# Kernel optimization log

Measured on AMD Instinct MI355X. Metric: run time of the kernel, lower is better.

The kernel has to match this reference:

```python
import jax, jax.numpy as jnp
import numpy as np

N0, N1, N2 = 100000, 20000, 4000   # src(block0), dst(block0)=src(block1), dst(block1)
R = 3                               # number of relations
E0, E1 = 160000, 64000              # edges per relation per block
IN_FEATS, HID = 128, 128
TSS, RS = 64, 64
NTOT = 200000                       # global node count for tss/rs embed tables
F_IN = HID + TSS + RS               # IGConv input feature dim = 256


def _lin(key, fi, fo):
    k1, k2 = jax.random.split(key)
    s = float(1.0 / np.sqrt(fi))
    w = jax.random.uniform(k1, (fi, fo), minval=-s, maxval=s, dtype=jnp.float32)
    b = jax.random.uniform(k2, (fo,), minval=-s, maxval=s, dtype=jnp.float32)
    return w, b


def setup_inputs() -> dict:
    ks = jax.random.split(jax.random.key(0), 32)
    inp = {}
    inp["x_user"] = jax.random.normal(ks[0], (N0, IN_FEATS), dtype=jnp.float32)
    inp["tss_embed"] = jax.random.normal(ks[1], (NTOT, TSS), dtype=jnp.float32)
    inp["rs_embed"] = jax.random.normal(ks[2], (NTOT, RS), dtype=jnp.float32)
    inp["src_nid0"] = jax.random.randint(ks[3], (N0,), 0, NTOT)
    inp["src_nid1"] = jax.random.randint(ks[4], (N1,), 0, NTOT)
    inp["e0_src"] = jax.random.randint(ks[5], (R, E0), 0, N0)
    inp["e0_dst"] = jax.random.randint(ks[6], (R, E0), 0, N1)
    inp["e1_src"] = jax.random.randint(ks[7], (R, E1), 0, N1)
    inp["e1_dst"] = jax.random.randint(ks[8], (R, E1), 0, N2)
    inp["embed_w"], inp["embed_b"] = _lin(ks[9], IN_FEATS, HID)
    i = 10
    for l in (1, 2):
        for nm, fi in (("fc1", F_IN), ("fc2", 3 * F_IN), ("fc3", 2 * HID)):
            pw, pb = zip(*[_lin(jax.random.fold_in(ks[i], r), fi, HID) for r in range(R)])
            inp["l%d_%s_w" % (l, nm)] = jnp.stack(pw)  # [R, fi, HID]
            inp["l%d_%s_b" % (l, nm)] = jnp.stack(pb)  # [R, HID]
            i += 1
    inp["attn_w1"], inp["attn_b1"] = _lin(ks[i], HID, HID)
    inp["attn_w2"] = _lin(ks[i + 1], HID, 1)[0]  # Linear(hid,1,bias=False)
    inp["pred_w"], inp["pred_b"] = _lin(ks[i + 2], HID, 1)
    return inp


def _igconv(src_feat, dst_feat, esrc, edst, n_dst, fc1w, fc1b, fc2w, fc2b, fc3w, fc3b):
    # copy_u gather then max/mean/sum segment reductions over destination nodes
    m = src_feat[esrc]                                   # [E, F]
    s = jax.ops.segment_sum(m, edst, num_segments=n_dst)
    deg = jax.ops.segment_sum(jnp.ones(esrc.shape, m.dtype), edst, num_segments=n_dst)
    mean = s / jnp.maximum(deg, 1.0)[:, None]
    mx = jax.ops.segment_max(m, edst, num_segments=n_dst)
    mx = jnp.where(deg[:, None] > 0, mx, jnp.zeros_like(mx))  # DGL zeros for isolated dst
    msg = jnp.concatenate([mx, mean, s], axis=1)         # [n_dst, 3F]
    inp = jnp.concatenate([msg @ fc2w + fc2b, dst_feat @ fc1w + fc1b], axis=1)
    return jax.nn.relu(inp) @ fc3w + fc3b                # [n_dst, HID]


def _attn(z, w1, b1, w2):
    # SemanticAttention: z [N, R, HID]
    w = (jnp.tanh(z @ w1 + b1) @ w2).mean(0)             # [R, 1]
    beta = jax.nn.softmax(w, axis=0)                     # [R, 1]
    return (beta[None] * z).sum(1)                       # [N, HID]


def _forward(x_user, tss_embed, rs_embed, embed_w, embed_b,
             l1_fc1_w, l1_fc1_b, l1_fc2_w, l1_fc2_b, l1_fc3_w, l1_fc3_b,
             l2_fc1_w, l2_fc1_b, l2_fc2_w, l2_fc2_b, l2_fc3_w, l2_fc3_b,
             attn_w1, attn_b1, attn_w2, pred_w, pred_b,
             src_nid0, src_nid1, e0_src, e0_dst, e1_src, e1_dst):
    u0 = x_user @ embed_w + embed_b                      # self.embed
    feat0 = jnp.concatenate([u0, tss_embed[src_nid0], rs_embed[src_nid0]], axis=1)  # [N0,256]
    conv1 = jax.vmap(lambda es, ed, w1, b1, w2, b2, w3, b3:
                     _igconv(feat0, feat0[:N1], es, ed, N1, w1, b1, w2, b2, w3, b3))
    z1 = conv1(e0_src, e0_dst, l1_fc1_w, l1_fc1_b, l1_fc2_w, l1_fc2_b, l1_fc3_w, l1_fc3_b)  # [R,N1,HID]
    h1 = jax.nn.relu(_attn(jnp.transpose(z1, (1, 0, 2)), attn_w1, attn_b1, attn_w2))  # [N1,HID]
    feat1 = jnp.concatenate([h1, tss_embed[src_nid1], rs_embed[src_nid1]], axis=1)    # [N1,256]
    conv2 = jax.vmap(lambda es, ed, w1, b1, w2, b2, w3, b3:
                     _igconv(feat1, feat1[:N2], es, ed, N2, w1, b1, w2, b2, w3, b3))
    z2 = conv2(e1_src, e1_dst, l2_fc1_w, l2_fc1_b, l2_fc2_w, l2_fc2_b, l2_fc3_w, l2_fc3_b)  # [R,N2,HID]
    h2 = _attn(jnp.transpose(z2, (1, 0, 2)), attn_w1, attn_b1, attn_w2)              # [N2,HID]
    return jax.nn.sigmoid(h2 @ pred_w + pred_b)          # [N2,1]


def reference(x_user, tss_embed, rs_embed, src_nid0, src_nid1,
              e0_src, e0_dst, e1_src, e1_dst, embed_w, embed_b,
              l1_fc1_w, l1_fc1_b, l1_fc2_w, l1_fc2_b, l1_fc3_w, l1_fc3_b,
              l2_fc1_w, l2_fc1_b, l2_fc2_w, l2_fc2_b, l2_fc3_w, l2_fc3_b,
              attn_w1, attn_b1, attn_w2, pred_w, pred_b):
    return _forward(x_user, tss_embed, rs_embed, embed_w, embed_b,
                    l1_fc1_w, l1_fc1_b, l1_fc2_w, l1_fc2_b, l1_fc3_w, l1_fc3_b,
                    l2_fc1_w, l2_fc1_b, l2_fc2_w, l2_fc2_b, l2_fc3_w, l2_fc3_b,
                    attn_w1, attn_b1, attn_w2, pred_w, pred_b,
                    src_nid0, src_nid1, e0_src, e0_dst, e1_src, e1_dst)
```

## Files before the change

### kernel.cpp

```cpp
#include <hip/hip_runtime.h>
#include <math.h>


typedef short s16x8 __attribute__((ext_vector_type(8)));
typedef float f32x4 __attribute__((ext_vector_type(4)));

__device__ __forceinline__ ushort f2bf(float f) {
  unsigned u = __float_as_uint(f);
  return (ushort)((u + 0x7FFFu + ((u >> 16) & 1u)) >> 16);
}
__device__ __forceinline__ float bf2f(unsigned hbits) {
  return __uint_as_float(hbits << 16);
}
__device__ __forceinline__ unsigned pack2(float lo, float hi) {
  return (unsigned)f2bf(lo) | ((unsigned)f2bf(hi) << 16);
}

struct PrepAll {
  const float* src[8];
  ushort* dst[8];
  int K[8];
  int total[8];
};

__global__ __launch_bounds__(256) void prep_all(PrepAll P)
{
  int t = blockIdx.z;
  int off = blockIdx.x * 256 + threadIdx.x;
  if (off >= P.total[t]) return;
  int K = P.K[t];
  int k = off % K;
  int n = (off / K) & 127;
  int r = off / (K * 128);
  P.dst[t][off] = f2bf(P.src[t][((size_t)r * K + k) * 128 + n]);
}

struct GemmDesc {
  const void* A; int lda; size_t aStride; int aKind;
  const ushort* Wt; size_t wStride;
  const float* bias; int biasStride;
  void* C; int ldc; size_t cStride; int cKind;
  int M, K, relu;
  const ushort* aggM; const ushort* aggS; const float* invdeg;
  size_t aggStride; int invStride;
  const int* gnid; const float* gtss; const float* grs;
};

template<int AKIND>
__device__ __forceinline__ uint4 loadA(const void* Ab, const ushort* AgM,
                                       const ushort* AgS, int lda, int row,
                                       bool rowOK, int k0, int quad, float idg)
{
  uint4 pk = make_uint4(0u, 0u, 0u, 0u);
  if (rowOK) {
    if constexpr (AKIND == 1) {
      pk = *(const uint4*)((const ushort*)Ab + (size_t)row * lda + k0 + quad * 8);
    } else if constexpr (AKIND == 0) {
      const float* A32 = (const float*)Ab;
      float4 fa = *(const float4*)(A32 + (size_t)row * lda + k0 + quad * 8);
      float4 fb = *(const float4*)(A32 + (size_t)row * lda + k0 + quad * 8 + 4);
      pk.x = pack2(fa.x, fa.y); pk.y = pack2(fa.z, fa.w);
      pk.z = pack2(fb.x, fb.y); pk.w = pack2(fb.z, fb.w);
    } else {
      int seg = k0 >> 8;
      int jj  = (k0 & 255) + quad * 8;
      const ushort* Ag = (seg == 0) ? AgM : AgS;
      pk = *(const uint4*)(Ag + (size_t)row * 256 + jj);
      if (seg == 1) {
        pk.x = pack2(bf2f(pk.x & 0xFFFFu) * idg, bf2f(pk.x >> 16) * idg);
        pk.y = pack2(bf2f(pk.y & 0xFFFFu) * idg, bf2f(pk.y >> 16) * idg);
        pk.z = pack2(bf2f(pk.z & 0xFFFFu) * idg, bf2f(pk.z >> 16) * idg);
        pk.w = pack2(bf2f(pk.w & 0xFFFFu) * idg, bf2f(pk.w >> 16) * idg);
      }
    }
  }
  return pk;
}

template<int K, int AKIND>
__device__ __forceinline__ void gemm_core(const GemmDesc& d, int r, ushort* Bs)
{
  constexpr int NC = K / 64;
  constexpr int NF = K / 32;

  const int tid = threadIdx.x;
  const int wave = tid >> 6, lane = tid & 63;
  const int m16 = lane & 15, quad = lane >> 4;
  const int rowBase = blockIdx.x * 64;
  const int row = rowBase + wave * 16 + m16;
  const bool rowOK = row < d.M;
  const ushort* Wt = d.Wt + (size_t)r * d.wStride;

  const void* Ab = (const char*)d.A +
      (size_t)r * d.aStride * (AKIND == 0 ? sizeof(float) : sizeof(ushort));
  const ushort* AgM = d.aggM + (size_t)r * d.aggStride;
  const ushort* AgS = d.aggS + (size_t)r * d.aggStride;

  float idg = 1.f;
  if (AKIND == 2 && rowOK) idg = d.invdeg[(size_t)r * d.invStride + row];

  f32x4 acc[8];
  #pragma unroll
  for (int j = 0; j < 8; ++j)
    #pragma unroll
    for (int p = 0; p < 4; ++p) acc[j][p] = 0.f;

  uint4 pkAll[(K <= 256) ? NF : 2];
  if constexpr (K <= 256) {
    #pragma unroll
    for (int f = 0; f < NF; ++f)
      pkAll[f] = loadA<AKIND>(Ab, AgM, AgS, d.lda, row, rowOK, f * 32, quad, idg);
  }

  #pragma unroll
  for (int c = 0; c < NC; ++c) {
    if constexpr (K > 256) {
      pkAll[0] = loadA<AKIND>(Ab, AgM, AgS, d.lda, row, rowOK, c * 64,      quad, idg);
      pkAll[1] = loadA<AKIND>(Ab, AgM, AgS, d.lda, row, rowOK, c * 64 + 32, quad, idg);
    }
    if (c) __syncthreads();
    #pragma unroll
    for (int i = 0; i < 4; ++i) {
      int q = tid + 256 * i;
      int col = ((q >> 6) & 7) * 16 + (q & 15);
      int kk  = c * 64 + (q >> 9) * 32 + ((q >> 4) & 3) * 8;
      *(uint4*)&Bs[q * 8] = *(const uint4*)(Wt + (size_t)col * K + kk);
    }
    __syncthreads();

    #pragma unroll
    for (int ks = 0; ks < 2; ++ks) {
      uint4 pk = (K <= 256) ? pkAll[c * 2 + ks] : pkAll[ks];
      s16x8 af = *(s16x8*)&pk;
      #pragma unroll
      for (int j = 0; j < 8; ++j) {
        s16x8 bf = *(const s16x8*)&Bs[((ks * 8 + j) * 64 + lane) * 8];
        acc[j] = __builtin_amdgcn_mfma_f32_16x16x32_bf16(af, bf, acc[j], 0, 0, 0);
      }
    }
  }

  const float* bias = d.bias + (size_t)r * d.biasStride;
  float bcol[8];
  #pragma unroll
  for (int j = 0; j < 8; ++j) bcol[j] = bias[j * 16 + m16];

  #pragma unroll
  for (int p = 0; p < 4; ++p) {
    int grow = rowBase + wave * 16 + quad * 4 + p;
    if (grow >= d.M) continue;
    if (d.cKind == 0) {
      float* Crow = (float*)d.C + (size_t)r * d.cStride + (size_t)grow * d.ldc;
      #pragma unroll
      for (int j = 0; j < 8; ++j) {
        float v = acc[j][p] + bcol[j];
        if (d.relu) v = fmaxf(v, 0.f);
        Crow[j * 16 + m16] = v;
      }
    } else {
      ushort* Crow = (ushort*)d.C + (size_t)r * d.cStride + (size_t)grow * d.ldc;
      #pragma unroll
      for (int j = 0; j < 8; ++j) {
        float v = acc[j][p] + bcol[j];
        if (d.relu) v = fmaxf(v, 0.f);
        Crow[j * 16 + m16] = f2bf(v);
      }
    }
  }

  if constexpr (K == 128) {
    if (d.gnid) {
      #pragma unroll
      for (int i = 0; i < 8; ++i) {
        int q = tid + 256 * i;
        int grow = rowBase + (q >> 5);
        int c = q & 31;
        if (grow >= d.M) continue;
        int id = d.gnid[grow];
        float4 v = (c < 16) ? *(const float4*)(d.gtss + (size_t)id * 64 + c * 4)
                            : *(const float4*)(d.grs  + (size_t)id * 64 + (c - 16) * 4);
        uint2 g; g.x = pack2(v.x, v.y); g.y = pack2(v.z, v.w);
        *(uint2*)((ushort*)d.C + (size_t)grow * d.ldc + 128 + c * 4) = g;
      }
    }
  }
}

__global__ __launch_bounds__(256, 4) void gemm_mfma(GemmDesc d0, GemmDesc d1)
{
  __shared__ __align__(16) ushort Bs[1024 * 8];
  const GemmDesc& d = blockIdx.z ? d1 : d0;
  const int r = blockIdx.y;
  if (d.K == 128)      gemm_core<128, 0>(d, r, Bs);
  else if (d.K == 256) gemm_core<256, 1>(d, r, Bs);
  else                 gemm_core<768, 2>(d, r, Bs);
}

__global__ __launch_bounds__(256, 4) void attn_mfma(
    const float* __restrict__ z, const ushort* __restrict__ w1t,
    const float* __restrict__ b1, const float* __restrict__ w2,
    int N, float* __restrict__ wsum)
{
  const int r = blockIdx.y;
  const float* zr = z + (size_t)r * N * 128;
  __shared__ __align__(16) ushort Bs[1024 * 8];

  const int tid = threadIdx.x;
  const int wave = tid >> 6, lane = tid & 63;
  const int m16 = lane & 15, quad = lane >> 4;
  const int rowBase = blockIdx.x * 64;
  const int row = rowBase + wave * 16 + m16;
  const bool rowOK = row < N;

  f32x4 acc[8];
  #pragma unroll
  for (int j = 0; j < 8; ++j)
    #pragma unroll
    for (int p = 0; p < 4; ++p) acc[j][p] = 0.f;

  uint4 pkAll[4];
  #pragma unroll
  for (int f = 0; f < 4; ++f) {
    uint4 pk = make_uint4(0u, 0u, 0u, 0u);
    if (rowOK) {
      float4 fa = *(const float4*)(zr + (size_t)row * 128 + f * 32 + quad * 8);
      float4 fb = *(const float4*)(zr + (size_t)row * 128 + f * 32 + quad * 8 + 4);
      pk.x = pack2(fa.x, fa.y); pk.y = pack2(fa.z, fa.w);
      pk.z = pack2(fb.x, fb.y); pk.w = pack2(fb.z, fb.w);
    }
    pkAll[f] = pk;
  }

  #pragma unroll
  for (int c = 0; c < 2; ++c) {
    if (c) __syncthreads();
    #pragma unroll
    for (int i = 0; i < 4; ++i) {
      int q = tid + 256 * i;
      int col = ((q >> 6) & 7) * 16 + (q & 15);
      int kk  = c * 64 + (q >> 9) * 32 + ((q >> 4) & 3) * 8;
      *(uint4*)&Bs[q * 8] = *(const uint4*)(w1t + (size_t)col * 128 + kk);
    }
    __syncthreads();

    #pragma unroll
    for (int ks = 0; ks < 2; ++ks) {
      s16x8 af = *(s16x8*)&pkAll[c * 2 + ks];
      #pragma unroll
      for (int j = 0; j < 8; ++j) {
        s16x8 bf = *(const s16x8*)&Bs[((ks * 8 + j) * 64 + lane) * 8];
        acc[j] = __builtin_amdgcn_mfma_f32_16x16x32_bf16(af, bf, acc[j], 0, 0, 0);
      }
    }
  }

  float b1c[8], w2c[8];
  #pragma unroll
  for (int j = 0; j < 8; ++j) { b1c[j] = b1[j * 16 + m16]; w2c[j] = w2[j * 16 + m16]; }

  float local = 0.f;
  #pragma unroll
  for (int p = 0; p < 4; ++p) {
    int grow = rowBase + wave * 16 + quad * 4 + p;
    if (grow >= N) continue;
    #pragma unroll
    for (int j = 0; j < 8; ++j)
      local += tanhf(acc[j][p] + b1c[j]) * w2c[j];
  }
  #pragma unroll
  for (int o = 32; o > 0; o >>= 1) local += __shfl_down(local, o);
  __shared__ float red[4];
  if (lane == 0) red[wave] = local;
  __syncthreads();
  if (tid == 0) atomicAdd(&wsum[r], red[0] + red[1] + red[2] + red[3]);
}

__global__ void count_deg(const int* __restrict__ edst, int E, int N, int* __restrict__ deg)
{
  int e = blockIdx.x * blockDim.x + threadIdx.x;
  int r = blockIdx.y;
  if (e < E) atomicAdd(&deg[r * N + edst[(size_t)r * E + e]], 1);
}

__global__ __launch_bounds__(1024) void scan_kernel(
    const int* __restrict__ deg, int* __restrict__ rowptr,
    int* __restrict__ cursor, int N)
{
  __shared__ int wtot[16];
  __shared__ int chunk_total_s;
  const int tid = threadIdx.x, lane = tid & 63, wid = tid >> 6;
  int running = 0;
  for (int base = 0; base < N; base += 4096) {
    int i0 = base + tid * 4;
    int d0 = 0, d1 = 0, d2 = 0, d3 = 0;
    if (i0 < N) {
      if (i0 + 3 < N) { int4 t = *(const int4*)(deg + i0); d0 = t.x; d1 = t.y; d2 = t.z; d3 = t.w; }
      else { d0 = deg[i0]; if (i0+1 < N) d1 = deg[i0+1]; if (i0+2 < N) d2 = deg[i0+2]; }
    }
    int tsum = d0 + d1 + d2 + d3;
    int incl = tsum;
    #pragma unroll
    for (int o = 1; o < 64; o <<= 1) {
      int t = __shfl_up(incl, o);
      if (lane >= o) incl += t;
    }
    if (lane == 63) wtot[wid] = incl;
    __syncthreads();
    if (wid == 0 && lane < 16) {
      int t = wtot[lane];
      int inc = t;
      #pragma unroll
      for (int o = 1; o < 16; o <<= 1) {
        int u = __shfl_up(inc, o);
        if (lane >= o) inc += u;
      }
      wtot[lane] = inc - t;
      if (lane == 15) chunk_total_s = inc;
    }
    __syncthreads();
    int excl = running + wtot[wid] + (incl - tsum);
    if (i0 < N) {
      int e1 = excl + d0, e2 = e1 + d1, e3 = e2 + d2;
      if (i0 + 3 < N) {
        *(int4*)(rowptr + i0) = make_int4(excl, e1, e2, e3);
        *(int4*)(cursor + i0) = make_int4(0, 0, 0, 0);
      } else {
        rowptr[i0] = excl; cursor[i0] = 0;
        if (i0+1 < N) { rowptr[i0+1] = e1; cursor[i0+1] = 0; }
        if (i0+2 < N) { rowptr[i0+2] = e2; cursor[i0+2] = 0; }
      }
    }
    running += chunk_total_s;
    __syncthreads();
  }
  if (tid == 0) rowptr[N] = running;
}

__global__ void fill_csr(const int* __restrict__ esrc, const int* __restrict__ edst,
                         int E, int N, const int* __restrict__ rowptr,
                         int* __restrict__ cursor, int* __restrict__ csr)
{
  int e = blockIdx.x * blockDim.x + threadIdx.x;
  int r = blockIdx.y;
  if (e >= E) return;
  int d = r * N + edst[(size_t)r * E + e];
  int pos = atomicAdd(&cursor[d], 1);
  csr[rowptr[d] + pos] = esrc[(size_t)r * E + e];
}

__global__ __launch_bounds__(256) void agg_kernel(
    const ushort* __restrict__ feat, const int* __restrict__ csr,
    const int* __restrict__ rowptr, int N, int c0, int cr, int CH,
    ushort* __restrict__ aggS, ushort* __restrict__ aggM, float* __restrict__ invdeg)
{
  const int wid = threadIdx.x >> 6, lane = threadIdx.x & 63;
  const int node = blockIdx.x * 4 + wid;
  if (node >= cr) return;
  const int g = blockIdx.y * N + c0 + node;
  const int o = blockIdx.y * CH + node;
  const int start = rowptr[g], end = rowptr[g + 1];
  const int j = lane * 4;
  float s0 = 0.f, s1 = 0.f, s2 = 0.f, s3 = 0.f;
  float m0 = -INFINITY, m1 = -INFINITY, m2 = -INFINITY, m3 = -INFINITY;
  int e = start;
  for (; e + 4 <= end; e += 4) {
    int sa = csr[e], sb = csr[e+1], sc = csr[e+2], sd = csr[e+3];
    uint2 va = *(const uint2*)(feat + (size_t)sa * 256 + j);
    uint2 vb = *(const uint2*)(feat + (size_t)sb * 256 + j);
    uint2 vc = *(const uint2*)(feat + (size_t)sc * 256 + j);
    uint2 vd = *(const uint2*)(feat + (size_t)sd * 256 + j);
    float a0, a1, a2, a3;
    a0 = bf2f(va.x & 0xFFFFu); a1 = bf2f(va.x >> 16); a2 = bf2f(va.y & 0xFFFFu); a3 = bf2f(va.y >> 16);
    s0 += a0; s1 += a1; s2 += a2; s3 += a3;
    m0 = fmaxf(m0, a0); m1 = fmaxf(m1, a1); m2 = fmaxf(m2, a2); m3 = fmaxf(m3, a3);
    a0 = bf2f(vb.x & 0xFFFFu); a1 = bf2f(vb.x >> 16); a2 = bf2f(vb.y & 0xFFFFu); a3 = bf2f(vb.y >> 16);
    s0 += a0; s1 += a1; s2 += a2; s3 += a3;
    m0 = fmaxf(m0, a0); m1 = fmaxf(m1, a1); m2 = fmaxf(m2, a2); m3 = fmaxf(m3, a3);
    a0 = bf2f(vc.x & 0xFFFFu); a1 = bf2f(vc.x >> 16); a2 = bf2f(vc.y & 0xFFFFu); a3 = bf2f(vc.y >> 16);
    s0 += a0; s1 += a1; s2 += a2; s3 += a3;
    m0 = fmaxf(m0, a0); m1 = fmaxf(m1, a1); m2 = fmaxf(m2, a2); m3 = fmaxf(m3, a3);
    a0 = bf2f(vd.x & 0xFFFFu); a1 = bf2f(vd.x >> 16); a2 = bf2f(vd.y & 0xFFFFu); a3 = bf2f(vd.y >> 16);
    s0 += a0; s1 += a1; s2 += a2; s3 += a3;
    m0 = fmaxf(m0, a0); m1 = fmaxf(m1, a1); m2 = fmaxf(m2, a2); m3 = fmaxf(m3, a3);
  }
  for (; e < end; ++e) {
    int src = csr[e];
    uint2 v = *(const uint2*)(feat + (size_t)src * 256 + j);
    float a0 = bf2f(v.x & 0xFFFFu), a1 = bf2f(v.x >> 16);
    float a2 = bf2f(v.y & 0xFFFFu), a3 = bf2f(v.y >> 16);
    s0 += a0; s1 += a1; s2 += a2; s3 += a3;
    m0 = fmaxf(m0, a0); m1 = fmaxf(m1, a1); m2 = fmaxf(m2, a2); m3 = fmaxf(m3, a3);
  }
  if (end == start) { m0 = m1 = m2 = m3 = 0.f; }
  uint2 ps; ps.x = pack2(s0, s1); ps.y = pack2(s2, s3);
  *(uint2*)(aggS + (size_t)o * 256 + j) = ps;
  uint2 pm; pm.x = pack2(m0, m1); pm.y = pack2(m2, m3);
  *(uint2*)(aggM + (size_t)o * 256 + j) = pm;
  if (lane == 0) invdeg[o] = 1.f / fmaxf((float)(end - start), 1.f);
}

__global__ void beta_kernel(const float* __restrict__ wsum, float invN, float* __restrict__ beta) {
  float w0 = wsum[0] * invN, w1 = wsum[1] * invN, w2 = wsum[2] * invN;
  float m  = fmaxf(w0, fmaxf(w1, w2));
  float e0 = expf(w0 - m), e1 = expf(w1 - m), e2 = expf(w2 - m);
  float s  = e0 + e1 + e2;
  beta[0] = e0 / s; beta[1] = e1 / s; beta[2] = e2 / s;
}

__global__ __launch_bounds__(256) void combine1_kernel(
    const float* __restrict__ z1, const float* __restrict__ beta,
    const float* __restrict__ tss, const float* __restrict__ rs,
    const int* __restrict__ nid, int N, ushort* __restrict__ feat1)
{
  int n = blockIdx.x, t = threadIdx.x;
  size_t NH = (size_t)N * 128;
  if (t < 128) {
    float v = beta[0] * z1[(size_t)n*128 + t] + beta[1] * z1[NH + (size_t)n*128 + t]
            + beta[2] * z1[2*NH + (size_t)n*128 + t];
    feat1[(size_t)n*256 + t] = f2bf(fmaxf(v, 0.f));
  } else {
    int j = t - 128;
    int id = nid[n];
    float v = (j < 64) ? tss[(size_t)id*64 + j] : rs[(size_t)id*64 + j - 64];
    feat1[(size_t)n*256 + t] = f2bf(v);
  }
}

__global__ __launch_bounds__(128) void combine2_pred(
    const float* __restrict__ z2, const float* __restrict__ beta, int N,
    const float* __restrict__ pw, const float* __restrict__ pb, float* __restrict__ out)
{
  int n = blockIdx.x, t = threadIdx.x;
  size_t NH = (size_t)N * 128;
  float h = beta[0] * z2[(size_t)n*128 + t] + beta[1] * z2[NH + (size_t)n*128 + t]
          + beta[2] * z2[2*NH + (size_t)n*128 + t];
  float p = h * pw[t];
  #pragma unroll
  for (int o = 32; o > 0; o >>= 1) p += __shfl_down(p, o);
  __shared__ float red[2];
  if ((t & 63) == 0) red[t >> 6] = p;
  __syncthreads();
  if (t == 0) {
    float v = red[0] + red[1] + pb[0];
    out[n] = 1.f / (1.f + expf(-v));
  }
}

extern "C" void kernel_launch(void* const* d_in, const int* in_sizes, int n_in,
                              void* d_out, int out_size, void* d_ws, size_t ws_size,
                              hipStream_t stream)
{
  const float* x_user  = (const float*)d_in[0];
  const float* tss     = (const float*)d_in[1];
  const float* rs      = (const float*)d_in[2];
  const int* src_nid0  = (const int*)d_in[3];
  const int* src_nid1  = (const int*)d_in[4];
  const int* e0_src    = (const int*)d_in[5];
  const int* e0_dst    = (const int*)d_in[6];
  const int* e1_src    = (const int*)d_in[7];
  const int* e1_dst    = (const int*)d_in[8];
  const float* embed_w = (const float*)d_in[9];
  const float* embed_b = (const float*)d_in[10];
  const float* l1w[3]  = {(const float*)d_in[11], (const float*)d_in[13], (const float*)d_in[15]};
  const float* l1b[3]  = {(const float*)d_in[12], (const float*)d_in[14], (const float*)d_in[16]};
  const float* l2w[3]  = {(const float*)d_in[17], (const float*)d_in[19], (const float*)d_in[21]};
  const float* l2b[3]  = {(const float*)d_in[18], (const float*)d_in[20], (const float*)d_in[22]};
  const float* attn_w1 = (const float*)d_in[23];
  const float* attn_b1 = (const float*)d_in[24];
  const float* attn_w2 = (const float*)d_in[25];
  const float* pred_w  = (const float*)d_in[26];
  const float* pred_b  = (const float*)d_in[27];
  float* out = (float*)d_out;

  const int N0 = in_sizes[0] / 128;
  const int N1 = in_sizes[4];
  const int N2 = out_size;
  const int E0 = in_sizes[5] / 3;
  const int E1 = in_sizes[7] / 3;

  char* wp = (char*)d_ws;
  auto walloc = [&](size_t bytes) {
    char* p = wp; wp += (bytes + 255) & ~(size_t)255; return p;
  };
  ushort* feat0  = (ushort*)walloc((size_t)N0 * 256 * 2);
  ushort* inp    = (ushort*)walloc((size_t)3 * N1 * 256 * 2);
  float*  z      = (float*)walloc((size_t)3 * N1 * 128 * 4);
  ushort* wt_emb = (ushort*)walloc((size_t)128 * 128 * 2);
  ushort* wt_attn = (ushort*)walloc((size_t)128 * 128 * 2);
  ushort* wt_fc1[2], *wt_fc2[2], *wt_fc3[2];
  for (int l = 0; l < 2; ++l) {
    wt_fc1[l] = (ushort*)walloc((size_t)3 * 256 * 128 * 2);
    wt_fc2[l] = (ushort*)walloc((size_t)3 * 768 * 128 * 2);
    wt_fc3[l] = (ushort*)walloc((size_t)3 * 256 * 128 * 2);
  }
  int*   degcnt = (int*)walloc((size_t)3 * N1 * 4);
  int*   rowptr = (int*)walloc((size_t)(3 * N1 + 1) * 4);
  int*   csr    = (int*)walloc((size_t)3 * E0 * 4);
  float* small  = (float*)walloc(256);
  float* wsum = small;
  float* beta = small + 4;
  ushort* feat1 = feat0;

  size_t used = (size_t)(wp - (char*)d_ws);
  size_t avail = (ws_size > used + 65536) ? (ws_size - used - 65536) : 0;
  const size_t per_row = (size_t)3 * (2 * 256 * 2 + 4 + 64);
  int CH = (int)(avail / per_row);
  if (CH > N1) CH = N1;
  if (CH < 1024) CH = 1024;
  ushort* aggS   = (ushort*)walloc((size_t)3 * CH * 256 * 2);
  ushort* aggM   = (ushort*)walloc((size_t)3 * CH * 256 * 2);
  float*  invdeg = (float*)walloc((size_t)3 * CH * 4);
  (void)n_in;

  {
    PrepAll P;
    P.src[0] = embed_w;  P.dst[0] = wt_emb;    P.K[0] = 128; P.total[0] = 128 * 128;
    P.src[1] = attn_w1;  P.dst[1] = wt_attn;   P.K[1] = 128; P.total[1] = 128 * 128;
    P.src[2] = l1w[0];   P.dst[2] = wt_fc1[0]; P.K[2] = 256; P.total[2] = 3 * 256 * 128;
    P.src[3] = l1w[1];   P.dst[3] = wt_fc2[0]; P.K[3] = 768; P.total[3] = 3 * 768 * 128;
    P.src[4] = l1w[2];   P.dst[4] = wt_fc3[0]; P.K[4] = 256; P.total[4] = 3 * 256 * 128;
    P.src[5] = l2w[0];   P.dst[5] = wt_fc1[1]; P.K[5] = 256; P.total[5] = 3 * 256 * 128;
    P.src[6] = l2w[1];   P.dst[6] = wt_fc2[1]; P.K[6] = 768; P.total[6] = 3 * 768 * 128;
    P.src[7] = l2w[2];   P.dst[7] = wt_fc3[1]; P.K[7] = 256; P.total[7] = 3 * 256 * 128;
    prep_all<<<dim3((3 * 768 * 128 + 255) / 256, 1, 8), 256, 0, stream>>>(P);
  }

  GemmDesc dz = {};
  dz.K = 256;

  {
    GemmDesc d{};
    d.A = x_user; d.lda = 128; d.aStride = 0; d.aKind = 0;
    d.Wt = wt_emb; d.wStride = 0; d.bias = embed_b; d.biasStride = 0;
    d.C = feat0; d.ldc = 256; d.cStride = 0; d.cKind = 1;
    d.M = N0; d.K = 128; d.relu = 0;
    d.aggM = aggM; d.aggS = aggS; d.invdeg = invdeg; d.aggStride = 0; d.invStride = 0;
    d.gnid = src_nid0; d.gtss = tss; d.grs = rs;
    gemm_mfma<<<dim3((N0 + 63) / 64, 1, 1), 256, 0, stream>>>(d, dz);
  }

  for (int layer = 0; layer < 2; ++layer) {
    const ushort* featS = layer ? feat1 : feat0;
    int Nd = layer ? N2 : N1;
    int E  = layer ? E1 : E0;
    const int* es = layer ? e1_src : e0_src;
    const int* ed = layer ? e1_dst : e0_dst;
    const float* const* lb = layer ? l2b : l1b;

    hipMemsetAsync(degcnt, 0, (size_t)3 * Nd * 4, stream);
    count_deg<<<dim3((E + 255) / 256, 3), 256, 0, stream>>>(ed, E, Nd, degcnt);
    scan_kernel<<<1, 1024, 0, stream>>>(degcnt, rowptr, degcnt, 3 * Nd);
    fill_csr<<<dim3((E + 255) / 256, 3), 256, 0, stream>>>(es, ed, E, Nd, rowptr, degcnt, csr);

    for (int c0 = 0; c0 < Nd; c0 += CH) {
      int cr = (Nd - c0 < CH) ? (Nd - c0) : CH;
      agg_kernel<<<dim3((cr + 3) / 4, 3), 256, 0, stream>>>(
          featS, csr, rowptr, Nd, c0, cr, CH, aggS, aggM, invdeg);
      GemmDesc d2{};
      d2.A = nullptr; d2.lda = 0; d2.aStride = 0; d2.aKind = 2;
      d2.Wt = wt_fc2[layer]; d2.wStride = (size_t)768 * 128; d2.bias = lb[1]; d2.biasStride = 128;
      d2.C = inp + (size_t)c0 * 256; d2.ldc = 256; d2.cStride = (size_t)Nd * 256; d2.cKind = 1;
      d2.M = cr; d2.K = 768; d2.relu = 1;
      d2.aggM = aggM; d2.aggS = aggS; d2.invdeg = invdeg;
      d2.aggStride = (size_t)CH * 256; d2.invStride = CH;
      GemmDesc d1{};
      d1.A = featS + (size_t)c0 * 256; d1.lda = 256; d1.aStride = 0; d1.aKind = 1;
      d1.Wt = wt_fc1[layer]; d1.wStride = (size_t)256 * 128; d1.bias = lb[0]; d1.biasStride = 128;
      d1.C = inp + 128 + (size_t)c0 * 256; d1.ldc = 256; d1.cStride = (size_t)Nd * 256; d1.cKind = 1;
      d1.M = cr; d1.K = 256; d1.relu = 1;
      d1.aggM = aggM; d1.aggS = aggS; d1.invdeg = invdeg; d1.aggStride = 0; d1.invStride = 0;
      gemm_mfma<<<dim3((cr + 63) / 64, 3, 2), 256, 0, stream>>>(d2, d1);
    }
    {
      GemmDesc d3{};
      d3.A = inp; d3.lda = 256; d3.aStride = (size_t)Nd * 256; d3.aKind = 1;
      d3.Wt = wt_fc3[layer]; d3.wStride = (size_t)256 * 128; d3.bias = lb[2]; d3.biasStride = 128;
      d3.C = z; d3.ldc = 128; d3.cStride = (size_t)Nd * 128; d3.cKind = 0;
      d3.M = Nd; d3.K = 256; d3.relu = 0;
      d3.aggM = aggM; d3.aggS = aggS; d3.invdeg = invdeg; d3.aggStride = 0; d3.invStride = 0;
      gemm_mfma<<<dim3((Nd + 63) / 64, 3, 1), 256, 0, stream>>>(d3, dz);
    }

    hipMemsetAsync(wsum, 0, 3 * sizeof(float), stream);
    attn_mfma<<<dim3((Nd + 63) / 64, 3), 256, 0, stream>>>(z, wt_attn, attn_b1, attn_w2, Nd, wsum);
    beta_kernel<<<1, 1, 0, stream>>>(wsum, 1.0f / (float)Nd, beta);

    if (layer == 0) {
      combine1_kernel<<<N1, 256, 0, stream>>>(z, beta, tss, rs, src_nid1, N1, feat1);
    } else {
      combine2_pred<<<N2, 128, 0, stream>>>(z, beta, N2, pred_w, pred_b, out);
    }
  }
}
```

Baseline: 551.1 us.

## Fuse fc3 GEMM with attention projection and parallelize CSR scan per relation

Merges the fc3 GEMM and the attention score GEMM into a single kernel. The fc3 output tile is kept in swizzled LDS as bf16 and fed straight into the attention MFMA, which avoids re-reading z from global memory and saves one launch. The CSR scan now runs as three independent blocks, one per relation, instead of one serial block over all relations. Rowptr and csr indices are made relation-local to support this. The fused kernel uses more shared memory and registers, and its bf16 rounding of z matches the previous pack path.

```diff
diff --git a/kernel.cpp b/kernel.cpp
--- a/kernel.cpp
+++ b/kernel.cpp
@@ -123,7 +123,7 @@
     for (int i = 0; i < 4; ++i) {
       int q = tid + 256 * i;
       int col = ((q >> 6) & 7) * 16 + (q & 15);
-      int kk  = c * 64 + (q >> 9) * 32 + ((q >> 4) & 3) * 8;
+      int kk  = c * 64 + ((q >> 9) & 1) * 32 + ((q >> 4) & 3) * 8;
       *(uint4*)&Bs[q * 8] = *(const uint4*)(Wt + (size_t)col * K + kk);
     }
     __syncthreads();
@@ -196,21 +196,27 @@
   else                 gemm_core<768, 2>(d, r, Bs);
 }
 
-__global__ __launch_bounds__(256, 4) void attn_mfma(
-    const float* __restrict__ z, const ushort* __restrict__ w1t,
-    const float* __restrict__ b1, const float* __restrict__ w2,
-    int N, float* __restrict__ wsum)
-{
-  const int r = blockIdx.y;
-  const float* zr = z + (size_t)r * N * 128;
-  __shared__ __align__(16) ushort Bs[1024 * 8];
+__global__ __launch_bounds__(256) void fc3_attn(
+    const ushort* __restrict__ inp, size_t aStride,
+    const ushort* __restrict__ wt3, size_t wStride,
+    const float* __restrict__ b3,
+    float* __restrict__ z, size_t zStride, int M,
+    const ushort* __restrict__ w1t, const float* __restrict__ b1,
+    const float* __restrict__ w2, float* __restrict__ wsum)
+{
+  __shared__ __align__(16) ushort Zs[64 * 128];
+  __shared__ __align__(16) ushort Ws[1024 * 8];
 
   const int tid = threadIdx.x;
   const int wave = tid >> 6, lane = tid & 63;
   const int m16 = lane & 15, quad = lane >> 4;
+  const int r = blockIdx.y;
   const int rowBase = blockIdx.x * 64;
   const int row = rowBase + wave * 16 + m16;
-  const bool rowOK = row < N;
+  const bool rowOK = row < M;
+
+  const ushort* A  = inp + (size_t)r * aStride;
+  const ushort* Wt = wt3 + (size_t)r * wStride;
 
   f32x4 acc[8];
   #pragma unroll
@@ -218,38 +224,85 @@
     #pragma unroll
     for (int p = 0; p < 4; ++p) acc[j][p] = 0.f;
 
-  uint4 pkAll[4];
-  #pragma unroll
-  for (int f = 0; f < 4; ++f) {
+  uint4 pkAll[8];
+  #pragma unroll
+  for (int f = 0; f < 8; ++f) {
     uint4 pk = make_uint4(0u, 0u, 0u, 0u);
-    if (rowOK) {
-      float4 fa = *(const float4*)(zr + (size_t)row * 128 + f * 32 + quad * 8);
-      float4 fb = *(const float4*)(zr + (size_t)row * 128 + f * 32 + quad * 8 + 4);
-      pk.x = pack2(fa.x, fa.y); pk.y = pack2(fa.z, fa.w);
-      pk.z = pack2(fb.x, fb.y); pk.w = pack2(fb.z, fb.w);
-    }
+    if (rowOK) pk = *(const uint4*)(A + (size_t)row * 256 + f * 32 + quad * 8);
     pkAll[f] = pk;
   }
 
   #pragma unroll
-  for (int c = 0; c < 2; ++c) {
+  for (int c = 0; c < 4; ++c) {
     if (c) __syncthreads();
     #pragma unroll
     for (int i = 0; i < 4; ++i) {
       int q = tid + 256 * i;
       int col = ((q >> 6) & 7) * 16 + (q & 15);
-      int kk  = c * 64 + (q >> 9) * 32 + ((q >> 4) & 3) * 8;
-      *(uint4*)&Bs[q * 8] = *(const uint4*)(w1t + (size_t)col * 128 + kk);
+      int kk  = c * 64 + ((q >> 9) & 1) * 32 + ((q >> 4) & 3) * 8;
+      *(uint4*)&Ws[q * 8] = *(const uint4*)(Wt + (size_t)col * 256 + kk);
     }
     __syncthreads();
-
     #pragma unroll
     for (int ks = 0; ks < 2; ++ks) {
       s16x8 af = *(s16x8*)&pkAll[c * 2 + ks];
       #pragma unroll
       for (int j = 0; j < 8; ++j) {
-        s16x8 bf = *(const s16x8*)&Bs[((ks * 8 + j) * 64 + lane) * 8];
+        s16x8 bf = *(const s16x8*)&Ws[((ks * 8 + j) * 64 + lane) * 8];
         acc[j] = __builtin_amdgcn_mfma_f32_16x16x32_bf16(af, bf, acc[j], 0, 0, 0);
+      }
+    }
+  }
+
+  const float* bias = b3 + (size_t)r * 128;
+  float bcol[8];
+  #pragma unroll
+  for (int j = 0; j < 8; ++j) bcol[j] = bias[j * 16 + m16];
+
+  #pragma unroll
+  for (int p = 0; p < 4; ++p) {
+    int lrow = wave * 16 + quad * 4 + p;
+    int grow = rowBase + lrow;
+    bool ok = grow < M;
+    float* Zr = z + (size_t)r * zStride + (size_t)grow * 128;
+    #pragma unroll
+    for (int j = 0; j < 8; ++j) {
+      float v = ok ? acc[j][p] + bcol[j] : 0.f;
+      if (ok) Zr[j * 16 + m16] = v;
+      int byte = lrow * 256 + (j * 16 + m16) * 2;
+      byte ^= (lrow & 7) << 4;
+      *(ushort*)((char*)Zs + byte) = f2bf(v);
+    }
+  }
+
+  f32x4 acc2[8];
+  #pragma unroll
+  for (int j = 0; j < 8; ++j)
+    #pragma unroll
+    for (int p = 0; p < 4; ++p) acc2[j][p] = 0.f;
+
+  const int arow = wave * 16 + m16;
+  #pragma unroll
+  for (int c = 0; c < 2; ++c) {
+    __syncthreads();
+    #pragma unroll
+    for (int i = 0; i < 4; ++i) {
+      int q = tid + 256 * i;
+      int col = ((q >> 6) & 7) * 16 + (q & 15);
+      int kk  = c * 64 + ((q >> 9) & 1) * 32 + ((q >> 4) & 3) * 8;
+      *(uint4*)&Ws[q * 8] = *(const uint4*)(w1t + (size_t)col * 128 + kk);
+    }
+    __syncthreads();
+    #pragma unroll
+    for (int ks = 0; ks < 2; ++ks) {
+      int kk = c * 64 + ks * 32 + quad * 8;
+      int byte = arow * 256 + kk * 2;
+      byte ^= (arow & 7) << 4;
+      s16x8 af = *(const s16x8*)((const char*)Zs + byte);
+      #pragma unroll
+      for (int j = 0; j < 8; ++j) {
+        s16x8 bf = *(const s16x8*)&Ws[((ks * 8 + j) * 64 + lane) * 8];
+        acc2[j] = __builtin_amdgcn_mfma_f32_16x16x32_bf16(af, bf, acc2[j], 0, 0, 0);
       }
     }
   }
@@ -262,10 +315,10 @@
   #pragma unroll
   for (int p = 0; p < 4; ++p) {
     int grow = rowBase + wave * 16 + quad * 4 + p;
-    if (grow >= N) continue;
+    if (grow >= M) continue;
     #pragma unroll
     for (int j = 0; j < 8; ++j)
-      local += tanhf(acc[j][p] + b1c[j]) * w2c[j];
+      local += tanhf(acc2[j][p] + b1c[j]) * w2c[j];
   }
   #pragma unroll
   for (int o = 32; o > 0; o >>= 1) local += __shfl_down(local, o);
@@ -286,6 +339,11 @@
     const int* __restrict__ deg, int* __restrict__ rowptr,
     int* __restrict__ cursor, int N)
 {
+  const int r = blockIdx.y;
+  const int* dg = deg + (size_t)r * N;
+  int* rp  = rowptr + (size_t)r * (N + 1);
+  int* cur = cursor + (size_t)r * N;
+
   __shared__ int wtot[16];
   __shared__ int chunk_total_s;
   const int tid = threadIdx.x, lane = tid & 63, wid = tid >> 6;
@@ -294,8 +352,8 @@
     int i0 = base + tid * 4;
     int d0 = 0, d1 = 0, d2 = 0, d3 = 0;
     if (i0 < N) {
-      if (i0 + 3 < N) { int4 t = *(const int4*)(deg + i0); d0 = t.x; d1 = t.y; d2 = t.z; d3 = t.w; }
-      else { d0 = deg[i0]; if (i0+1 < N) d1 = deg[i0+1]; if (i0+2 < N) d2 = deg[i0+2]; }
+      if (i0 + 3 < N) { int4 t = *(const int4*)(dg + i0); d0 = t.x; d1 = t.y; d2 = t.z; d3 = t.w; }
+      else { d0 = dg[i0]; if (i0+1 < N) d1 = dg[i0+1]; if (i0+2 < N) d2 = dg[i0+2]; }
     }
     int tsum = d0 + d1 + d2 + d3;
     int incl = tsum;
@@ -322,18 +380,18 @@
     if (i0 < N) {
       int e1 = excl + d0, e2 = e1 + d1, e3 = e2 + d2;
       if (i0 + 3 < N) {
-        *(int4*)(rowptr + i0) = make_int4(excl, e1, e2, e3);
-        *(int4*)(cursor + i0) = make_int4(0, 0, 0, 0);
+        *(int4*)(rp + i0) = make_int4(excl, e1, e2, e3);
+        *(int4*)(cur + i0) = make_int4(0, 0, 0, 0);
       } else {
-        rowptr[i0] = excl; cursor[i0] = 0;
-        if (i0+1 < N) { rowptr[i0+1] = e1; cursor[i0+1] = 0; }
-        if (i0+2 < N) { rowptr[i0+2] = e2; cursor[i0+2] = 0; }
+        rp[i0] = excl; cur[i0] = 0;
+        if (i0+1 < N) { rp[i0+1] = e1; cur[i0+1] = 0; }
+        if (i0+2 < N) { rp[i0+2] = e2; cur[i0+2] = 0; }
       }
     }
     running += chunk_total_s;
     __syncthreads();
   }
-  if (tid == 0) rowptr[N] = running;
+  if (tid == 0) rp[N] = running;
 }
 
 __global__ void fill_csr(const int* __restrict__ esrc, const int* __restrict__ edst,
@@ -343,28 +401,29 @@
   int e = blockIdx.x * blockDim.x + threadIdx.x;
   int r = blockIdx.y;
   if (e >= E) return;
-  int d = r * N + edst[(size_t)r * E + e];
-  int pos = atomicAdd(&cursor[d], 1);
-  csr[rowptr[d] + pos] = esrc[(size_t)r * E + e];
+  int dn = edst[(size_t)r * E + e];
+  int pos = atomicAdd(&cursor[r * N + dn], 1);
+  csr[(size_t)r * E + rowptr[(size_t)r * (N + 1) + dn] + pos] = esrc[(size_t)r * E + e];
 }
 
 __global__ __launch_bounds__(256) void agg_kernel(
     const ushort* __restrict__ feat, const int* __restrict__ csr,
-    const int* __restrict__ rowptr, int N, int c0, int cr, int CH,
+    const int* __restrict__ rowptr, int N, int c0, int cr, int CH, int E,
     ushort* __restrict__ aggS, ushort* __restrict__ aggM, float* __restrict__ invdeg)
 {
   const int wid = threadIdx.x >> 6, lane = threadIdx.x & 63;
   const int node = blockIdx.x * 4 + wid;
   if (node >= cr) return;
-  const int g = blockIdx.y * N + c0 + node;
+  const size_t rp = (size_t)blockIdx.y * (N + 1) + c0 + node;
   const int o = blockIdx.y * CH + node;
-  const int start = rowptr[g], end = rowptr[g + 1];
+  const int start = rowptr[rp], end = rowptr[rp + 1];
+  const int* ecsr = csr + (size_t)blockIdx.y * E;
   const int j = lane * 4;
   float s0 = 0.f, s1 = 0.f, s2 = 0.f, s3 = 0.f;
   float m0 = -INFINITY, m1 = -INFINITY, m2 = -INFINITY, m3 = -INFINITY;
   int e = start;
   for (; e + 4 <= end; e += 4) {
-    int sa = csr[e], sb = csr[e+1], sc = csr[e+2], sd = csr[e+3];
+    int sa = ecsr[e], sb = ecsr[e+1], sc = ecsr[e+2], sd = ecsr[e+3];
     uint2 va = *(const uint2*)(feat + (size_t)sa * 256 + j);
     uint2 vb = *(const uint2*)(feat + (size_t)sb * 256 + j);
     uint2 vc = *(const uint2*)(feat + (size_t)sc * 256 + j);
@@ -384,7 +443,7 @@
     m0 = fmaxf(m0, a0); m1 = fmaxf(m1, a1); m2 = fmaxf(m2, a2); m3 = fmaxf(m3, a3);
   }
   for (; e < end; ++e) {
-    int src = csr[e];
+    int src = ecsr[e];
     uint2 v = *(const uint2*)(feat + (size_t)src * 256 + j);
     float a0 = bf2f(v.x & 0xFFFFu), a1 = bf2f(v.x >> 16);
     float a2 = bf2f(v.y & 0xFFFFu), a3 = bf2f(v.y >> 16);
@@ -494,7 +553,7 @@
     wt_fc3[l] = (ushort*)walloc((size_t)3 * 256 * 128 * 2);
   }
   int*   degcnt = (int*)walloc((size_t)3 * N1 * 4);
-  int*   rowptr = (int*)walloc((size_t)(3 * N1 + 1) * 4);
+  int*   rowptr = (int*)walloc((size_t)3 * (N1 + 1) * 4);
   int*   csr    = (int*)walloc((size_t)3 * E0 * 4);
   float* small  = (float*)walloc(256);
   float* wsum = small;
@@ -549,13 +608,13 @@
 
     hipMemsetAsync(degcnt, 0, (size_t)3 * Nd * 4, stream);
     count_deg<<<dim3((E + 255) / 256, 3), 256, 0, stream>>>(ed, E, Nd, degcnt);
-    scan_kernel<<<1, 1024, 0, stream>>>(degcnt, rowptr, degcnt, 3 * Nd);
+    scan_kernel<<<dim3(1, 3), 1024, 0, stream>>>(degcnt, rowptr, degcnt, Nd);
     fill_csr<<<dim3((E + 255) / 256, 3), 256, 0, stream>>>(es, ed, E, Nd, rowptr, degcnt, csr);
 
     for (int c0 = 0; c0 < Nd; c0 += CH) {
       int cr = (Nd - c0 < CH) ? (Nd - c0) : CH;
       agg_kernel<<<dim3((cr + 3) / 4, 3), 256, 0, stream>>>(
-          featS, csr, rowptr, Nd, c0, cr, CH, aggS, aggM, invdeg);
+          featS, csr, rowptr, Nd, c0, cr, CH, E, aggS, aggM, invdeg);
       GemmDesc d2{};
       d2.A = nullptr; d2.lda = 0; d2.aStride = 0; d2.aKind = 2;
       d2.Wt = wt_fc2[layer]; d2.wStride = (size_t)768 * 128; d2.bias = lb[1]; d2.biasStride = 128;
@@ -571,18 +630,11 @@
       d1.aggM = aggM; d1.aggS = aggS; d1.invdeg = invdeg; d1.aggStride = 0; d1.invStride = 0;
       gemm_mfma<<<dim3((cr + 63) / 64, 3, 2), 256, 0, stream>>>(d2, d1);
     }
-    {
-      GemmDesc d3{};
-      d3.A = inp; d3.lda = 256; d3.aStride = (size_t)Nd * 256; d3.aKind = 1;
-      d3.Wt = wt_fc3[layer]; d3.wStride = (size_t)256 * 128; d3.bias = lb[2]; d3.biasStride = 128;
-      d3.C = z; d3.ldc = 128; d3.cStride = (size_t)Nd * 128; d3.cKind = 0;
-      d3.M = Nd; d3.K = 256; d3.relu = 0;
-      d3.aggM = aggM; d3.aggS = aggS; d3.invdeg = invdeg; d3.aggStride = 0; d3.invStride = 0;
-      gemm_mfma<<<dim3((Nd + 63) / 64, 3, 1), 256, 0, stream>>>(d3, dz);
-    }
 
     hipMemsetAsync(wsum, 0, 3 * sizeof(float), stream);
-    attn_mfma<<<dim3((Nd + 63) / 64, 3), 256, 0, stream>>>(z, wt_attn, attn_b1, attn_w2, Nd, wsum);
+    fc3_attn<<<dim3((Nd + 63) / 64, 3), 256, 0, stream>>>(
+        inp, (size_t)Nd * 256, wt_fc3[layer], (size_t)256 * 128, lb[2],
+        z, (size_t)Nd * 128, Nd, wt_attn, attn_b1, attn_w2, wsum);
     beta_kernel<<<1, 1, 0, stream>>>(wsum, 1.0f / (float)Nd, beta);
 
     if (layer == 0) {
```

Result: faster. 522.5 us (-5.2%).
